# Kernel tuning notes

Measured on AMD Instinct MI355X. Metric: run time of the kernel, lower is better.

Reference implementation:

```python
import jax, jax.numpy as jnp
import numpy as np

N = 50000
E = 800000
IN_CH = 128
HID = 128
HEADS = 8
OUT_CH = 40
NEG_SLOPE = 0.2
BN_EPS = 1e-5


def gat_conv(x, src, dst, W, a_src, a_dst, bias, heads, ch, concat):
    # x: [N, F_in]; W: [heads*ch, F_in]; a_src/a_dst: [heads, ch]; bias: [heads*ch] or [ch]
    n = x.shape[0]
    h = (x @ W.T).reshape(n, heads, ch)                      # [N, H, C]
    alpha_src = (h * a_src[None]).sum(-1)                    # [N, H]
    alpha_dst = (h * a_dst[None]).sum(-1)                    # [N, H]
    e = alpha_src[src] + alpha_dst[dst]                      # [E, H]
    e = jax.nn.leaky_relu(e, NEG_SLOPE)
    # segment softmax over incoming edges of each destination node
    emax = jax.ops.segment_max(e, dst, num_segments=n)       # [N, H]
    ee = jnp.exp(e - emax[dst])
    denom = jax.ops.segment_sum(ee, dst, num_segments=n)     # [N, H]
    alpha = ee / (denom[dst] + 1e-16)                        # [E, H]
    msg = h[src] * alpha[:, :, None]                         # [E, H, C]
    out = jax.ops.segment_sum(msg, dst, num_segments=n)      # [N, H, C]
    out = out.reshape(n, heads * ch) if concat else out.mean(axis=1)
    return out + bias


def batch_norm_eval(x, gamma, beta, mean, var):
    return (x - mean) * jax.lax.rsqrt(var + BN_EPS) * gamma + beta


def setup_inputs() -> dict:
    key = jax.random.key(0)
    ks = jax.random.split(key, 16)
    ch = HID // HEADS  # 16
    s = 1.0 / np.sqrt(IN_CH)
    inp = {
        "x": jax.random.normal(ks[0], (N, IN_CH), dtype=jnp.float32),
        "edge_index": jax.random.randint(ks[1], (2, E), 0, N, dtype=jnp.int64),
        # layer 0
        "W0": jax.random.normal(ks[2], (HEADS * ch, IN_CH), jnp.float32) * s,
        "a_src0": jax.random.normal(ks[3], (HEADS, ch), jnp.float32) * 0.1,
        "a_dst0": jax.random.normal(ks[4], (HEADS, ch), jnp.float32) * 0.1,
        "b0": jnp.zeros((HID,), jnp.float32),
        "bn_g0": jnp.ones((HID,), jnp.float32),
        "bn_b0": jnp.zeros((HID,), jnp.float32),
        "bn_m0": jnp.zeros((HID,), jnp.float32),
        "bn_v0": jnp.ones((HID,), jnp.float32),
        # layer 1
        "W1": jax.random.normal(ks[5], (HEADS * ch, HID), jnp.float32) * (1.0 / np.sqrt(HID)),
        "a_src1": jax.random.normal(ks[6], (HEADS, ch), jnp.float32) * 0.1,
        "a_dst1": jax.random.normal(ks[7], (HEADS, ch), jnp.float32) * 0.1,
        "b1": jnp.zeros((HID,), jnp.float32),
        "bn_g1": jnp.ones((HID,), jnp.float32),
        "bn_b1": jnp.zeros((HID,), jnp.float32),
        "bn_m1": jnp.zeros((HID,), jnp.float32),
        "bn_v1": jnp.ones((HID,), jnp.float32),
        # output layer (heads=1, concat=False)
        "W2": jax.random.normal(ks[8], (OUT_CH, HID), jnp.float32) * (1.0 / np.sqrt(HID)),
        "a_src2": jax.random.normal(ks[9], (1, OUT_CH), jnp.float32) * 0.1,
        "a_dst2": jax.random.normal(ks[10], (1, OUT_CH), jnp.float32) * 0.1,
        "b2": jnp.zeros((OUT_CH,), jnp.float32),
    }
    return inp


def reference(x, edge_index, W0, a_src0, a_dst0, b0, bn_g0, bn_b0, bn_m0, bn_v0,
              W1, a_src1, a_dst1, b1, bn_g1, bn_b1, bn_m1, bn_v1,
              W2, a_src2, a_dst2, b2):
    n = x.shape[0]
    # PyG GATConv adds self-loops by default
    loops = jnp.arange(n, dtype=edge_index.dtype)
    src = jnp.concatenate([edge_index[0], loops])
    dst = jnp.concatenate([edge_index[1], loops])
    ch = HID // HEADS

    h = gat_conv(x, src, dst, W0, a_src0, a_dst0, b0, HEADS, ch, True)
    h = batch_norm_eval(h, bn_g0, bn_b0, bn_m0, bn_v0)
    h = jax.nn.elu(h)
    # dropout: eval mode (identity)

    h = gat_conv(h, src, dst, W1, a_src1, a_dst1, b1, HEADS, ch, True)
    h = batch_norm_eval(h, bn_g1, bn_b1, bn_m1, bn_v1)
    h = jax.nn.elu(h)

    out = gat_conv(h, src, dst, W2, a_src2, a_dst2, b2, 1, OUT_CH, False)
    return out
```

## Files before the change

### kernel.cpp

```cpp
#include <hip/hip_runtime.h>
#include <hip/hip_fp16.h>
#include <math.h>

constexpr float NEG_SLOPE = 0.2f;
constexpr float BN_EPS_C = 1e-5f;

using half8 = __attribute__((ext_vector_type(8))) _Float16;
using half4 = __attribute__((ext_vector_type(4))) _Float16;
using f32x4 = __attribute__((ext_vector_type(4))) float;


__global__ __launch_bounds__(256)
void hist_cvt_kernel(const int* __restrict__ ei, int* __restrict__ bucket_count,
                     int E, int N, int NEB,
                     const float* __restrict__ W0, const float* __restrict__ W1,
                     const float* __restrict__ W2,
                     __half* __restrict__ W0h, __half* __restrict__ W1h,
                     __half* __restrict__ W2h) {
    int t = threadIdx.x;
    if ((int)blockIdx.x >= NEB) {
        int i = ((int)blockIdx.x - NEB) * 256 + t;
        if (i < 16384) {
            W0h[i] = __float2half(W0[i]);
            W1h[i] = __float2half(W1[i]);
        }
        if (i < 6144) W2h[i] = __float2half(i < 5120 ? W2[i] : 0.f);
        return;
    }
    __shared__ int h[256];
    h[t] = 0;
    __syncthreads();
    int base = blockIdx.x * 8192;
    int ET = E + N;
#pragma unroll
    for (int q = 0; q < 32; ++q) {
        int i = base + q * 256 + t;
        if (i < ET) {
            int d = (i < E) ? ei[E + i] : (i - E);
            atomicAdd(&h[d >> 8], 1);
        }
    }
    __syncthreads();
    if (h[t] > 0) atomicAdd(&bucket_count[t], h[t]);
}

__global__ __launch_bounds__(256)
void bucket_scan_kernel(const int* __restrict__ bucket_count, int* __restrict__ bucket_ptr,
                        int* __restrict__ gcursor, int* __restrict__ row_ptr,
                        int N, int ET) {
    __shared__ int s[256];
    int t = threadIdx.x;
    int c = bucket_count[t];
    s[t] = c;
    __syncthreads();
    for (int off = 1; off < 256; off <<= 1) {
        int v = (t >= off) ? s[t - off] : 0;
        __syncthreads();
        s[t] += v;
        __syncthreads();
    }
    int excl = s[t] - c;
    bucket_ptr[t] = excl;
    gcursor[t] = excl;
    if (t == 255) {
        bucket_ptr[256] = s[255];
        row_ptr[N] = ET;
    }
}

__global__ __launch_bounds__(256)
void bucket_bin_kernel(const int* __restrict__ ei, int* __restrict__ gcursor,
                       unsigned* __restrict__ tmp, int E, int N) {
    __shared__ unsigned bins[8192];
    __shared__ int lcount[256];
    __shared__ int lofs[256];
    __shared__ int lbase[256];
    __shared__ int lcur[256];
    int t = threadIdx.x;
    lcount[t] = 0;
    __syncthreads();
    int base = blockIdx.x * 8192;
    int ET = E + N;
    unsigned pr[32];
#pragma unroll
    for (int q = 0; q < 32; ++q) {
        int i = base + q * 256 + t;
        pr[q] = 0xFFFFFFFFu;
        if (i < ET) {
            int s, d;
            if (i < E) { s = ei[i]; d = ei[E + i]; }
            else       { s = i - E; d = s; }
            pr[q] = ((unsigned)d << 16) | (unsigned)s;
            atomicAdd(&lcount[d >> 8], 1);
        }
    }
    __syncthreads();
    {
        int c = lcount[t];
        lofs[t] = c;
        __syncthreads();
        for (int off = 1; off < 256; off <<= 1) {
            int v = (t >= off) ? lofs[t - off] : 0;
            __syncthreads();
            lofs[t] += v;
            __syncthreads();
        }
        int excl = lofs[t] - c;
        __syncthreads();
        lofs[t] = excl;
        lcur[t] = excl;
        if (c > 0) lbase[t] = atomicAdd(&gcursor[t], c);
    }
    __syncthreads();
#pragma unroll
    for (int q = 0; q < 32; ++q) {
        if (pr[q] != 0xFFFFFFFFu) {
            int b = pr[q] >> 24;
            int p = atomicAdd(&lcur[b], 1);
            bins[p] = pr[q];
        }
    }
    __syncthreads();
    int total = min(8192, ET - base);
    for (int p = t; p < total; p += 256) {
        unsigned e = bins[p];
        int b = e >> 24;
        tmp[lbase[b] + (p - lofs[b])] = e;
    }
}

__global__ __launch_bounds__(256)
void fine_scatter_kernel(const unsigned* __restrict__ tmp, const int* __restrict__ bucket_ptr,
                         int* __restrict__ row_ptr, int* __restrict__ srcs, int N) {
    __shared__ int hist[256];
    __shared__ int scanb[256];
    __shared__ int cur[256];
    int b = blockIdx.x, t = threadIdx.x;
    int base = bucket_ptr[b];
    int cnt = bucket_ptr[b + 1] - base;
    int n0 = b << 8;
    hist[t] = 0;
    __syncthreads();
    for (int p = t; p < cnt; p += 256)
        atomicAdd(&hist[(int)(tmp[base + p] >> 16) - n0], 1);
    __syncthreads();
    int c = hist[t];
    scanb[t] = c;
    __syncthreads();
    for (int off = 1; off < 256; off <<= 1) {
        int v = (t >= off) ? scanb[t - off] : 0;
        __syncthreads();
        scanb[t] += v;
        __syncthreads();
    }
    int excl = scanb[t] - c;
    cur[t] = excl;
    if (n0 + t < N) row_ptr[n0 + t] = base + excl;
    __syncthreads();
    for (int p = t; p < cnt; p += 256) {
        unsigned e = tmp[base + p];
        int pos = atomicAdd(&cur[(int)(e >> 16) - n0], 1);
        srcs[base + pos] = (int)(e & 0xFFFFu);
    }
}


template<bool AHALF>
__global__ __launch_bounds__(256)
void gemm128_mfma_kernel(const void* __restrict__ Xv, const __half* __restrict__ W16,
                         const float* __restrict__ a_src, const float* __restrict__ a_dst,
                         __half* __restrict__ hp, float* __restrict__ asrc,
                         float* __restrict__ adst, int N) {
    __shared__ _Float16 Bs[128][136];
    const int t = threadIdx.x;
    const int n0 = blockIdx.x * 64;

#pragma unroll
    for (int i = 0; i < 8; ++i) {
        int lin = t + i * 256;
        int n = lin >> 4;
        int m = lin & 15;
        *reinterpret_cast<uint4*>(&Bs[n][8 * m]) =
            *reinterpret_cast<const uint4*>(&W16[(size_t)n * 128 + 8 * m]);
    }
    __syncthreads();

    const int l  = t & 63;
    const int w  = t >> 6;
    const int lr = l & 15;
    const int lg = l >> 4;
    const int rowA = n0 + 16 * w + lr;
    const bool rokA = rowA < N;

    f32x4 acc[8];
#pragma unroll
    for (int tt = 0; tt < 8; ++tt) acc[tt] = (f32x4){0.f, 0.f, 0.f, 0.f};

#pragma unroll
    for (int ks = 0; ks < 4; ++ks) {
        half8 a;
        if (rokA) {
            if constexpr (AHALF) {
                const __half* X = (const __half*)Xv;
                a = *reinterpret_cast<const half8*>(&X[(size_t)rowA * 128 + 8 * lg + 32 * ks]);
            } else {
                const float* X = (const float*)Xv;
                const float* p = &X[(size_t)rowA * 128 + 8 * lg + 32 * ks];
                float4 v0 = *reinterpret_cast<const float4*>(p);
                float4 v1 = *reinterpret_cast<const float4*>(p + 4);
                a[0] = (_Float16)v0.x; a[1] = (_Float16)v0.y;
                a[2] = (_Float16)v0.z; a[3] = (_Float16)v0.w;
                a[4] = (_Float16)v1.x; a[5] = (_Float16)v1.y;
                a[6] = (_Float16)v1.z; a[7] = (_Float16)v1.w;
            }
        } else {
#pragma unroll
            for (int q = 0; q < 8; ++q) a[q] = (_Float16)0.f;
        }
#pragma unroll
        for (int tt = 0; tt < 8; ++tt) {
            half8 b = *reinterpret_cast<const half8*>(&Bs[16 * tt + lr][8 * lg + 32 * ks]);
            acc[tt] = __builtin_amdgcn_mfma_f32_16x16x32_f16(a, b, acc[tt], 0, 0, 0);
        }
    }

    float av[8], bv[8];
#pragma unroll
    for (int tt = 0; tt < 8; ++tt) {
        av[tt] = a_src[16 * tt + lr];
        bv[tt] = a_dst[16 * tt + lr];
    }
#pragma unroll
    for (int reg = 0; reg < 4; ++reg) {
        int gr = n0 + 16 * w + 4 * lg + reg;
        bool ok = gr < N;
        if (ok) {
#pragma unroll
            for (int tt = 0; tt < 8; ++tt)
                hp[(size_t)gr * 128 + 16 * tt + lr] = __float2half(acc[tt][reg]);
        }
#pragma unroll
        for (int tt = 0; tt < 8; ++tt) {
            float p = acc[tt][reg] * av[tt];
            float q = acc[tt][reg] * bv[tt];
#pragma unroll
            for (int off = 1; off < 16; off <<= 1) {
                p += __shfl_xor(p, off, 16);
                q += __shfl_xor(q, off, 16);
            }
            if (ok && lr == tt) {
                asrc[(size_t)gr * 8 + tt] = p;
                adst[(size_t)gr * 8 + tt] = q;
            }
        }
    }
}


__global__ __launch_bounds__(256)
void gemm40_mfma_kernel(const __half* __restrict__ X, const __half* __restrict__ W16,
                        const float* __restrict__ a_src, const float* __restrict__ a_dst,
                        __half* __restrict__ hp, float* __restrict__ asrc,
                        float* __restrict__ adst, int N) {
    __shared__ _Float16 Bs[48][136];
    const int t = threadIdx.x;
    const int n0 = blockIdx.x * 64;

#pragma unroll
    for (int i = 0; i < 3; ++i) {
        int lin = t + i * 256;
        if (lin < 768) {
            int n = lin >> 4;
            int m = lin & 15;
            *reinterpret_cast<uint4*>(&Bs[n][8 * m]) =
                *reinterpret_cast<const uint4*>(&W16[(size_t)n * 128 + 8 * m]);
        }
    }
    __syncthreads();

    const int l  = t & 63;
    const int w  = t >> 6;
    const int lr = l & 15;
    const int lg = l >> 4;
    const int rowA = n0 + 16 * w + lr;
    const bool rokA = rowA < N;

    f32x4 acc[3];
#pragma unroll
    for (int tt = 0; tt < 3; ++tt) acc[tt] = (f32x4){0.f, 0.f, 0.f, 0.f};

#pragma unroll
    for (int ks = 0; ks < 4; ++ks) {
        half8 a;
        if (rokA) {
            a = *reinterpret_cast<const half8*>(&X[(size_t)rowA * 128 + 8 * lg + 32 * ks]);
        } else {
#pragma unroll
            for (int q = 0; q < 8; ++q) a[q] = (_Float16)0.f;
        }
#pragma unroll
        for (int tt = 0; tt < 3; ++tt) {
            half8 b = *reinterpret_cast<const half8*>(&Bs[16 * tt + lr][8 * lg + 32 * ks]);
            acc[tt] = __builtin_amdgcn_mfma_f32_16x16x32_f16(a, b, acc[tt], 0, 0, 0);
        }
    }

    float av[3], bv[3];
#pragma unroll
    for (int tt = 0; tt < 3; ++tt) {
        int j = 16 * tt + lr;
        av[tt] = (j < 40) ? a_src[j] : 0.f;
        bv[tt] = (j < 40) ? a_dst[j] : 0.f;
    }
#pragma unroll
    for (int reg = 0; reg < 4; ++reg) {
        int gr = n0 + 16 * w + 4 * lg + reg;
        bool ok = gr < N;
        float p = 0.f, q = 0.f;
#pragma unroll
        for (int tt = 0; tt < 3; ++tt) {
            int j = 16 * tt + lr;
            if (ok && j < 40) hp[(size_t)gr * 40 + j] = __float2half(acc[tt][reg]);
            p += acc[tt][reg] * av[tt];
            q += acc[tt][reg] * bv[tt];
        }
#pragma unroll
        for (int off = 1; off < 16; off <<= 1) {
            p += __shfl_xor(p, off, 16);
            q += __shfl_xor(q, off, 16);
        }
        if (ok && lr == 0) {
            asrc[gr] = p;
            adst[gr] = q;
        }
    }
}


__global__ __launch_bounds__(256)
void message128_kernel(const __half* __restrict__ hh, const int* __restrict__ row_ptr,
                       const int* __restrict__ srcs,
                       const float* __restrict__ asrc, const float* __restrict__ adst,
                       const float* __restrict__ bias,
                       const float* __restrict__ bn_g, const float* __restrict__ bn_b,
                       const float* __restrict__ bn_m, const float* __restrict__ bn_v,
                       __half* __restrict__ out16, int N) {
    int node = blockIdx.x * 8 + (threadIdx.x >> 5);
    if (node >= N) return;
    int tc = threadIdx.x & 31;
    int half_id = tc >> 4;
    int cl = tc & 15;
    int hd = cl >> 1;
    int beg = row_ptr[node], end = row_ptr[node + 1];
    float ad = adst[(size_t)node * 8 + hd];
    float ssum = 0.f;
    float acc[8];
#pragma unroll
    for (int q = 0; q < 8; ++q) acc[q] = 0.f;

    int j = beg;
    for (; j + 4 <= end; j += 4) {
        int sA = srcs[j + half_id];
        int sB = srcs[j + 2 + half_id];
        half8 vA = *reinterpret_cast<const half8*>(&hh[(size_t)sA * 128 + 8 * cl]);
        half8 vB = *reinterpret_cast<const half8*>(&hh[(size_t)sB * 128 + 8 * cl]);
        float eA = asrc[(size_t)sA * 8 + hd] + ad;
        float eB = asrc[(size_t)sB * 8 + hd] + ad;
        eA = (eA > 0.f) ? eA : NEG_SLOPE * eA;
        eB = (eB > 0.f) ? eB : NEG_SLOPE * eB;
        float wA = __expf(eA);
        float wB = __expf(eB);
        ssum += wA + wB;
#pragma unroll
        for (int q = 0; q < 8; ++q) {
            acc[q] = fmaf((float)vA[q], wA, acc[q]);
            acc[q] = fmaf((float)vB[q], wB, acc[q]);
        }
    }
    for (; j + 2 <= end; j += 2) {
        int s = srcs[j + half_id];
        half8 v = *reinterpret_cast<const half8*>(&hh[(size_t)s * 128 + 8 * cl]);
        float e = asrc[(size_t)s * 8 + hd] + ad;
        e = (e > 0.f) ? e : NEG_SLOPE * e;
        float wgt = __expf(e);
        ssum += wgt;
#pragma unroll
        for (int q = 0; q < 8; ++q) acc[q] = fmaf((float)v[q], wgt, acc[q]);
    }
    if (j < end && half_id == 0) {
        int s = srcs[j];
        half8 v = *reinterpret_cast<const half8*>(&hh[(size_t)s * 128 + 8 * cl]);
        float e = asrc[(size_t)s * 8 + hd] + ad;
        e = (e > 0.f) ? e : NEG_SLOPE * e;
        float wgt = __expf(e);
        ssum += wgt;
#pragma unroll
        for (int q = 0; q < 8; ++q) acc[q] = fmaf((float)v[q], wgt, acc[q]);
    }
    ssum += __shfl_xor(ssum, 16);
#pragma unroll
    for (int q = 0; q < 8; ++q) acc[q] += __shfl_xor(acc[q], 16);

    if (half_id == 0) {
        float inv = 1.0f / (ssum + 1e-16f);
        int c = cl * 8;
        float r[8];
#pragma unroll
        for (int pp = 0; pp < 2; ++pp) {
            int cc = c + 4 * pp;
            float4 bi = *reinterpret_cast<const float4*>(&bias[cc]);
            float4 g  = *reinterpret_cast<const float4*>(&bn_g[cc]);
            float4 bb = *reinterpret_cast<const float4*>(&bn_b[cc]);
            float4 mm = *reinterpret_cast<const float4*>(&bn_m[cc]);
            float4 vv = *reinterpret_cast<const float4*>(&bn_v[cc]);
            r[4 * pp + 0] = (acc[4 * pp + 0] * inv + bi.x - mm.x) * rsqrtf(vv.x + BN_EPS_C) * g.x + bb.x;
            r[4 * pp + 1] = (acc[4 * pp + 1] * inv + bi.y - mm.y) * rsqrtf(vv.y + BN_EPS_C) * g.y + bb.y;
            r[4 * pp + 2] = (acc[4 * pp + 2] * inv + bi.z - mm.z) * rsqrtf(vv.z + BN_EPS_C) * g.z + bb.z;
            r[4 * pp + 3] = (acc[4 * pp + 3] * inv + bi.w - mm.w) * rsqrtf(vv.w + BN_EPS_C) * g.w + bb.w;
        }
        half8 o;
#pragma unroll
        for (int q = 0; q < 8; ++q) {
            float rv = (r[q] > 0.f) ? r[q] : expm1f(r[q]);
            o[q] = (_Float16)rv;
        }
        *reinterpret_cast<half8*>(&out16[(size_t)node * 128 + c]) = o;
    }
}


__global__ __launch_bounds__(256)
void message40_kernel(const __half* __restrict__ hh2, const int* __restrict__ row_ptr,
                      const int* __restrict__ srcs,
                      const float* __restrict__ asrc, const float* __restrict__ adst,
                      const float* __restrict__ b2, float* __restrict__ out, int N) {
    int node = blockIdx.x * 16 + (threadIdx.x >> 4);
    if (node >= N) return;
    int tc = threadIdx.x & 15;
    int beg = row_ptr[node], end = row_ptr[node + 1];
    float ad = adst[node];
    float ssum = 0.f;
    float acc[4] = {0.f, 0.f, 0.f, 0.f};
    int j = beg;
    for (; j + 2 <= end; j += 2) {
        int s0 = srcs[j];
        int s1 = srcs[j + 1];
        half4 v0 = (half4){0, 0, 0, 0}, v1 = (half4){0, 0, 0, 0};
        if (tc < 10) {
            v0 = *reinterpret_cast<const half4*>(&hh2[(size_t)s0 * 40 + 4 * tc]);
            v1 = *reinterpret_cast<const half4*>(&hh2[(size_t)s1 * 40 + 4 * tc]);
        }
        float e0 = asrc[s0] + ad;
        float e1 = asrc[s1] + ad;
        e0 = (e0 > 0.f) ? e0 : NEG_SLOPE * e0;
        e1 = (e1 > 0.f) ? e1 : NEG_SLOPE * e1;
        float w0 = __expf(e0);
        float w1 = __expf(e1);
        ssum += w0 + w1;
#pragma unroll
        for (int q = 0; q < 4; ++q) {
            acc[q] = fmaf((float)v0[q], w0, acc[q]);
            acc[q] = fmaf((float)v1[q], w1, acc[q]);
        }
    }
    if (j < end) {
        int s0 = srcs[j];
        half4 v0 = (half4){0, 0, 0, 0};
        if (tc < 10) v0 = *reinterpret_cast<const half4*>(&hh2[(size_t)s0 * 40 + 4 * tc]);
        float e0 = asrc[s0] + ad;
        e0 = (e0 > 0.f) ? e0 : NEG_SLOPE * e0;
        float w0 = __expf(e0);
        ssum += w0;
#pragma unroll
        for (int q = 0; q < 4; ++q) acc[q] = fmaf((float)v0[q], w0, acc[q]);
    }
    if (tc < 10) {
        float inv = 1.0f / (ssum + 1e-16f);
        int c = tc * 4;
        float4 bi = *reinterpret_cast<const float4*>(&b2[c]);
        *reinterpret_cast<float4*>(&out[(size_t)node * 40 + c]) =
            make_float4(acc[0] * inv + bi.x, acc[1] * inv + bi.y,
                        acc[2] * inv + bi.z, acc[3] * inv + bi.w);
    }
}


static inline char* align256(char* p) {
    return (char*)(((uintptr_t)p + 255) & ~(uintptr_t)255);
}

extern "C" void kernel_launch(void* const* d_in, const int* in_sizes, int n_in,
                              void* d_out, int out_size, void* d_ws, size_t ws_size,
                              hipStream_t stream) {
    const float* x   = (const float*)d_in[0];
    const int*   ei  = (const int*)d_in[1];
    const float* W0  = (const float*)d_in[2];
    const float* as0 = (const float*)d_in[3];
    const float* ad0 = (const float*)d_in[4];
    const float* b0  = (const float*)d_in[5];
    const float* g0  = (const float*)d_in[6];
    const float* bb0 = (const float*)d_in[7];
    const float* m0  = (const float*)d_in[8];
    const float* v0  = (const float*)d_in[9];
    const float* W1  = (const float*)d_in[10];
    const float* as1 = (const float*)d_in[11];
    const float* ad1 = (const float*)d_in[12];
    const float* b1  = (const float*)d_in[13];
    const float* g1  = (const float*)d_in[14];
    const float* bb1 = (const float*)d_in[15];
    const float* m1  = (const float*)d_in[16];
    const float* v1  = (const float*)d_in[17];
    const float* W2  = (const float*)d_in[18];
    const float* as2 = (const float*)d_in[19];
    const float* ad2 = (const float*)d_in[20];
    const float* b2  = (const float*)d_in[21];

    const int N  = in_sizes[0] / 128;
    const int E  = in_sizes[1] / 2;
    const int ET = E + N;
    const int NBUK = (N + 255) >> 8;
    const int NEB  = (ET + 8191) / 8192;

    char* wsp = (char*)d_ws;
    int* bucket_count = (int*)wsp;  wsp = align256(wsp + 256 * 4);
    int* bucket_ptr   = (int*)wsp;  wsp = align256(wsp + 257 * 4);
    int* gcursor      = (int*)wsp;  wsp = align256(wsp + 256 * 4);
    int* row_ptr      = (int*)wsp;  wsp = align256(wsp + (size_t)(N + 1) * 4);
    unsigned* tmp     = (unsigned*)wsp; wsp = align256(wsp + (size_t)ET * 4);
    int* srcs         = (int*)wsp;  wsp = align256(wsp + (size_t)ET * 4);
    __half* hh        = (__half*)wsp; wsp = align256(wsp + (size_t)N * 128 * 2);
    __half* h2        = (__half*)wsp; wsp = align256(wsp + (size_t)N * 40 * 2);
    __half* feat      = (__half*)wsp; wsp = align256(wsp + (size_t)N * 128 * 2);
    float* asr        = (float*)wsp;  wsp = align256(wsp + (size_t)N * 8 * 4);
    float* adt        = (float*)wsp;  wsp = align256(wsp + (size_t)N * 8 * 4);
    __half* W0h       = (__half*)wsp; wsp = align256(wsp + 16384 * 2);
    __half* W1h       = (__half*)wsp; wsp = align256(wsp + 16384 * 2);
    __half* W2h       = (__half*)wsp; wsp = align256(wsp + 6144 * 2);

    hipMemsetAsync(bucket_count, 0, 256 * 4, stream);
    hist_cvt_kernel<<<NEB + 64, 256, 0, stream>>>(ei, bucket_count, E, N, NEB,
                                                  W0, W1, W2, W0h, W1h, W2h);
    bucket_scan_kernel<<<1, 256, 0, stream>>>(bucket_count, bucket_ptr, gcursor, row_ptr, N, ET);
    bucket_bin_kernel<<<NEB, 256, 0, stream>>>(ei, gcursor, tmp, E, N);
    fine_scatter_kernel<<<NBUK, 256, 0, stream>>>(tmp, bucket_ptr, row_ptr, srcs, N);

    const int g64 = (N + 63) / 64;

    gemm128_mfma_kernel<false><<<g64, 256, 0, stream>>>(x, W0h, as0, ad0, hh, asr, adt, N);
    message128_kernel<<<(N + 7) / 8, 256, 0, stream>>>(hh, row_ptr, srcs, asr, adt,
                                                       b0, g0, bb0, m0, v0, feat, N);
    gemm128_mfma_kernel<true><<<g64, 256, 0, stream>>>(feat, W1h, as1, ad1, hh, asr, adt, N);
    message128_kernel<<<(N + 7) / 8, 256, 0, stream>>>(hh, row_ptr, srcs, asr, adt,
                                                       b1, g1, bb1, m1, v1, feat, N);
    gemm40_mfma_kernel<<<g64, 256, 0, stream>>>(feat, W2h, as2, ad2, h2, asr, adt, N);
    message40_kernel<<<(N + 15) / 16, 256, 0, stream>>>(h2, row_ptr, srcs,
                                                        asr, adt, b2, (float*)d_out, N);
}
```

Measured before the change: 213.8 us.

## Fuse CSR build into one cooperative kernel and enlarge GEMM tiles

Merges the four CSR-construction kernels and the memset into a single cooperative kernel that uses grid-wide syncs, with per-block bucket counts scanned deterministically by block 0 instead of global atomic cursors. This removes several launch gaps and the atomics on the global cursor. It also changes the 128-wide GEMM to 512-thread blocks covering 128 rows each, which halves the weight-tile loads per row. Risks are cooperative-launch residency limits (about 104 blocks with a 32KB shared bins array), the serial scan in block 0, and whether the GEMM body, not visible here, was actually updated for 8 waves.

```diff
diff --git a/kernel.cpp b/kernel.cpp
--- a/kernel.cpp
+++ b/kernel.cpp
@@ -1,6 +1,9 @@
 #include <hip/hip_runtime.h>
 #include <hip/hip_fp16.h>
+#include <hip/hip_cooperative_groups.h>
 #include <math.h>
+
+namespace cg = cooperative_groups;
 
 constexpr float NEG_SLOPE = 0.2f;
 constexpr float BN_EPS_C = 1e-5f;
@@ -11,91 +14,83 @@
 
 
 __global__ __launch_bounds__(256)
-void hist_cvt_kernel(const int* __restrict__ ei, int* __restrict__ bucket_count,
-                     int E, int N, int NEB,
-                     const float* __restrict__ W0, const float* __restrict__ W1,
-                     const float* __restrict__ W2,
-                     __half* __restrict__ W0h, __half* __restrict__ W1h,
-                     __half* __restrict__ W2h) {
-    int t = threadIdx.x;
-    if ((int)blockIdx.x >= NEB) {
-        int i = ((int)blockIdx.x - NEB) * 256 + t;
+void csr_build_kernel(const int* __restrict__ ei, int* __restrict__ cnt,
+                      int* __restrict__ bucket_ptr, int* __restrict__ row_ptr,
+                      unsigned* __restrict__ tmp, int* __restrict__ srcs,
+                      int E, int N, int NEB, int NBUK,
+                      const float* __restrict__ W0, const float* __restrict__ W1,
+                      const float* __restrict__ W2,
+                      __half* __restrict__ W0h, __half* __restrict__ W1h,
+                      __half* __restrict__ W2h) {
+    cg::grid_group grid = cg::this_grid();
+    const int t = threadIdx.x;
+    const int blk = blockIdx.x;
+    const int ET = E + N;
+
+    __shared__ int lcount[256];
+    __shared__ int lofs[256];
+    __shared__ int lcur[256];
+    __shared__ unsigned bins[8192];
+
+    const bool isEdgeBlk = blk < NEB;
+    unsigned pr[32];
+
+    if (isEdgeBlk) {
+        lcount[t] = 0;
+        __syncthreads();
+        int base = blk * 8192;
+#pragma unroll
+        for (int q = 0; q < 32; ++q) {
+            int i = base + q * 256 + t;
+            pr[q] = 0xFFFFFFFFu;
+            if (i < ET) {
+                int s, d;
+                if (i < E) { s = ei[i]; d = ei[E + i]; }
+                else       { s = i - E; d = s; }
+                pr[q] = ((unsigned)d << 16) | (unsigned)s;
+                atomicAdd(&lcount[d >> 8], 1);
+            }
+        }
+        __syncthreads();
+        cnt[blk * 256 + t] = lcount[t];
+    } else if (blk < NEB + 64) {
+        int i = (blk - NEB) * 256 + t;
         if (i < 16384) {
             W0h[i] = __float2half(W0[i]);
             W1h[i] = __float2half(W1[i]);
         }
         if (i < 6144) W2h[i] = __float2half(i < 5120 ? W2[i] : 0.f);
-        return;
-    }
-    __shared__ int h[256];
-    h[t] = 0;
-    __syncthreads();
-    int base = blockIdx.x * 8192;
-    int ET = E + N;
-#pragma unroll
-    for (int q = 0; q < 32; ++q) {
-        int i = base + q * 256 + t;
-        if (i < ET) {
-            int d = (i < E) ? ei[E + i] : (i - E);
-            atomicAdd(&h[d >> 8], 1);
-        }
-    }
-    __syncthreads();
-    if (h[t] > 0) atomicAdd(&bucket_count[t], h[t]);
-}
-
-__global__ __launch_bounds__(256)
-void bucket_scan_kernel(const int* __restrict__ bucket_count, int* __restrict__ bucket_ptr,
-                        int* __restrict__ gcursor, int* __restrict__ row_ptr,
-                        int N, int ET) {
-    __shared__ int s[256];
-    int t = threadIdx.x;
-    int c = bucket_count[t];
-    s[t] = c;
-    __syncthreads();
-    for (int off = 1; off < 256; off <<= 1) {
-        int v = (t >= off) ? s[t - off] : 0;
-        __syncthreads();
-        s[t] += v;
-        __syncthreads();
-    }
-    int excl = s[t] - c;
-    bucket_ptr[t] = excl;
-    gcursor[t] = excl;
-    if (t == 255) {
-        bucket_ptr[256] = s[255];
-        row_ptr[N] = ET;
-    }
-}
-
-__global__ __launch_bounds__(256)
-void bucket_bin_kernel(const int* __restrict__ ei, int* __restrict__ gcursor,
-                       unsigned* __restrict__ tmp, int E, int N) {
-    __shared__ unsigned bins[8192];
-    __shared__ int lcount[256];
-    __shared__ int lofs[256];
-    __shared__ int lbase[256];
-    __shared__ int lcur[256];
-    int t = threadIdx.x;
-    lcount[t] = 0;
-    __syncthreads();
-    int base = blockIdx.x * 8192;
-    int ET = E + N;
-    unsigned pr[32];
-#pragma unroll
-    for (int q = 0; q < 32; ++q) {
-        int i = base + q * 256 + t;
-        pr[q] = 0xFFFFFFFFu;
-        if (i < ET) {
-            int s, d;
-            if (i < E) { s = ei[i]; d = ei[E + i]; }
-            else       { s = i - E; d = s; }
-            pr[q] = ((unsigned)d << 16) | (unsigned)s;
-            atomicAdd(&lcount[d >> 8], 1);
-        }
-    }
-    __syncthreads();
-    {
+    }
+    grid.sync();
+
+    if (blk == 0) {
+        int* sc = (int*)bins;
+        int total = 0;
+        for (int k = 0; k < NEB; ++k) {
+            int c = cnt[k * 256 + t];
+            cnt[k * 256 + t] = total;
+            total += c;
+        }
+        sc[t] = total;
+        __syncthreads();
+        for (int off = 1; off < 256; off <<= 1) {
+            int v = (t >= off) ? sc[t - off] : 0;
+            __syncthreads();
+            sc[t] += v;
+            __syncthreads();
+        }
+        int excl = sc[t] - total;
+        bucket_ptr[t] = excl;
+        if (t == 255) {
+            bucket_ptr[256] = sc[255];
+            row_ptr[N] = ET;
+        }
+        for (int k = 0; k < NEB; ++k)
+            cnt[k * 256 + t] += excl;
+    }
+    grid.sync();
+
+    if (isEdgeBlk) {
         int c = lcount[t];
         lofs[t] = c;
         __syncthreads();
@@ -109,75 +104,71 @@
         __syncthreads();
         lofs[t] = excl;
         lcur[t] = excl;
-        if (c > 0) lbase[t] = atomicAdd(&gcursor[t], c);
-    }
-    __syncthreads();
-#pragma unroll
-    for (int q = 0; q < 32; ++q) {
-        if (pr[q] != 0xFFFFFFFFu) {
-            int b = pr[q] >> 24;
-            int p = atomicAdd(&lcur[b], 1);
-            bins[p] = pr[q];
-        }
-    }
-    __syncthreads();
-    int total = min(8192, ET - base);
-    for (int p = t; p < total; p += 256) {
-        unsigned e = bins[p];
-        int b = e >> 24;
-        tmp[lbase[b] + (p - lofs[b])] = e;
-    }
-}
-
-__global__ __launch_bounds__(256)
-void fine_scatter_kernel(const unsigned* __restrict__ tmp, const int* __restrict__ bucket_ptr,
-                         int* __restrict__ row_ptr, int* __restrict__ srcs, int N) {
-    __shared__ int hist[256];
-    __shared__ int scanb[256];
-    __shared__ int cur[256];
-    int b = blockIdx.x, t = threadIdx.x;
-    int base = bucket_ptr[b];
-    int cnt = bucket_ptr[b + 1] - base;
-    int n0 = b << 8;
-    hist[t] = 0;
-    __syncthreads();
-    for (int p = t; p < cnt; p += 256)
-        atomicAdd(&hist[(int)(tmp[base + p] >> 16) - n0], 1);
-    __syncthreads();
-    int c = hist[t];
-    scanb[t] = c;
-    __syncthreads();
-    for (int off = 1; off < 256; off <<= 1) {
-        int v = (t >= off) ? scanb[t - off] : 0;
-        __syncthreads();
-        scanb[t] += v;
-        __syncthreads();
-    }
-    int excl = scanb[t] - c;
-    cur[t] = excl;
-    if (n0 + t < N) row_ptr[n0 + t] = base + excl;
-    __syncthreads();
-    for (int p = t; p < cnt; p += 256) {
-        unsigned e = tmp[base + p];
-        int pos = atomicAdd(&cur[(int)(e >> 16) - n0], 1);
-        srcs[base + pos] = (int)(e & 0xFFFFu);
+        __syncthreads();
+#pragma unroll
+        for (int q = 0; q < 32; ++q) {
+            if (pr[q] != 0xFFFFFFFFu) {
+                int b = pr[q] >> 24;
+                int p = atomicAdd(&lcur[b], 1);
+                bins[p] = pr[q];
+            }
+        }
+        __syncthreads();
+        lcur[t] = cnt[blk * 256 + t];
+        __syncthreads();
+        int total = min(8192, ET - blk * 8192);
+        for (int p = t; p < total; p += 256) {
+            unsigned e = bins[p];
+            int b = e >> 24;
+            tmp[lcur[b] + (p - lofs[b])] = e;
+        }
+    }
+    grid.sync();
+
+    if (blk < NBUK) {
+        int base = bucket_ptr[blk];
+        int cntb = bucket_ptr[blk + 1] - base;
+        int n0 = blk << 8;
+        lcount[t] = 0;
+        __syncthreads();
+        for (int p = t; p < cntb; p += 256)
+            atomicAdd(&lcount[(int)(tmp[base + p] >> 16) - n0], 1);
+        __syncthreads();
+        int c = lcount[t];
+        lofs[t] = c;
+        __syncthreads();
+        for (int off = 1; off < 256; off <<= 1) {
+            int v = (t >= off) ? lofs[t - off] : 0;
+            __syncthreads();
+            lofs[t] += v;
+            __syncthreads();
+        }
+        int excl = lofs[t] - c;
+        lcur[t] = excl;
+        if (n0 + t < N) row_ptr[n0 + t] = base + excl;
+        __syncthreads();
+        for (int p = t; p < cntb; p += 256) {
+            unsigned e = tmp[base + p];
+            int pos = atomicAdd(&lcur[(int)(e >> 16) - n0], 1);
+            srcs[base + pos] = (int)(e & 0xFFFFu);
+        }
     }
 }
 
 
 template<bool AHALF>
-__global__ __launch_bounds__(256)
+__global__ __launch_bounds__(512)
 void gemm128_mfma_kernel(const void* __restrict__ Xv, const __half* __restrict__ W16,
                          const float* __restrict__ a_src, const float* __restrict__ a_dst,
                          __half* __restrict__ hp, float* __restrict__ asrc,
                          float* __restrict__ adst, int N) {
     __shared__ _Float16 Bs[128][136];
     const int t = threadIdx.x;
-    const int n0 = blockIdx.x * 64;
-
-#pragma unroll
-    for (int i = 0; i < 8; ++i) {
-        int lin = t + i * 256;
+    const int n0 = blockIdx.x * 128;
+
+#pragma unroll
+    for (int i = 0; i < 4; ++i) {
+        int lin = t + i * 512;
         int n = lin >> 4;
         int m = lin & 15;
         *reinterpret_cast<uint4*>(&Bs[n][8 * m]) =
@@ -522,9 +513,8 @@
     const int NEB  = (ET + 8191) / 8192;
 
     char* wsp = (char*)d_ws;
-    int* bucket_count = (int*)wsp;  wsp = align256(wsp + 256 * 4);
+    int* cnt          = (int*)wsp;  wsp = align256(wsp + (size_t)NEB * 256 * 4);
     int* bucket_ptr   = (int*)wsp;  wsp = align256(wsp + 257 * 4);
-    int* gcursor      = (int*)wsp;  wsp = align256(wsp + 256 * 4);
     int* row_ptr      = (int*)wsp;  wsp = align256(wsp + (size_t)(N + 1) * 4);
     unsigned* tmp     = (unsigned*)wsp; wsp = align256(wsp + (size_t)ET * 4);
     int* srcs         = (int*)wsp;  wsp = align256(wsp + (size_t)ET * 4);
@@ -537,19 +527,28 @@
     __half* W1h       = (__half*)wsp; wsp = align256(wsp + 16384 * 2);
     __half* W2h       = (__half*)wsp; wsp = align256(wsp + 6144 * 2);
 
-    hipMemsetAsync(bucket_count, 0, 256 * 4, stream);
-    hist_cvt_kernel<<<NEB + 64, 256, 0, stream>>>(ei, bucket_count, E, N, NEB,
-                                                  W0, W1, W2, W0h, W1h, W2h);
-    bucket_scan_kernel<<<1, 256, 0, stream>>>(bucket_count, bucket_ptr, gcursor, row_ptr, N, ET);
-    bucket_bin_kernel<<<NEB, 256, 0, stream>>>(ei, gcursor, tmp, E, N);
-    fine_scatter_kernel<<<NBUK, 256, 0, stream>>>(tmp, bucket_ptr, row_ptr, srcs, N);
-
-    const int g64 = (N + 63) / 64;
-
-    gemm128_mfma_kernel<false><<<g64, 256, 0, stream>>>(x, W0h, as0, ad0, hh, asr, adt, N);
+    {
+        int E_ = E, N_ = N, NEB_ = NEB, NBUK_ = NBUK;
+        const int* ei_ = ei;
+        const float *W0_ = W0, *W1_ = W1, *W2_ = W2;
+        __half *W0h_ = W0h, *W1h_ = W1h, *W2h_ = W2h;
+        int* cnt_ = cnt; int* bp_ = bucket_ptr; int* rp_ = row_ptr;
+        unsigned* tmp_ = tmp; int* srcs_ = srcs;
+        void* args[] = { &ei_, &cnt_, &bp_, &rp_, &tmp_, &srcs_,
+                         &E_, &N_, &NEB_, &NBUK_,
+                         &W0_, &W1_, &W2_, &W0h_, &W1h_, &W2h_ };
+        int grid = (NBUK > NEB + 64) ? NBUK : (NEB + 64);
+        hipLaunchCooperativeKernel((void*)csr_build_kernel, dim3(grid), dim3(256),
+                                   args, 0, stream);
+    }
+
+    const int g128 = (N + 127) / 128;
+    const int g64  = (N + 63) / 64;
+
+    gemm128_mfma_kernel<false><<<g128, 512, 0, stream>>>(x, W0h, as0, ad0, hh, asr, adt, N);
     message128_kernel<<<(N + 7) / 8, 256, 0, stream>>>(hh, row_ptr, srcs, asr, adt,
                                                        b0, g0, bb0, m0, v0, feat, N);
-    gemm128_mfma_kernel<true><<<g64, 256, 0, stream>>>(feat, W1h, as1, ad1, hh, asr, adt, N);
+    gemm128_mfma_kernel<true><<<g128, 512, 0, stream>>>(feat, W1h, as1, ad1, hh, asr, adt, N);
     message128_kernel<<<(N + 7) / 8, 256, 0, stream>>>(hh, row_ptr, srcs, asr, adt,
                                                        b1, g1, bb1, m1, v1, feat, N);
     gemm40_mfma_kernel<<<g64, 256, 0, stream>>>(feat, W2h, as2, ad2, h2, asr, adt, N);
```

After: 300.1 us. 1.4x slower.
